# Performance work log

Hardware: AMD Instinct MI355X
Metric: run time of the kernel (lower is better)

## Reference

```python
import jax, jax.numpy as jnp
import numpy as np

NEG = -10000.0
START_ID, END_ID, PAD_ID = 0, 1, 2
B, S, T = 512, 512, 128


def setup_inputs() -> dict:
    key = jax.random.key(0)
    k1, k2, k3, k4 = jax.random.split(key, 4)
    x = jax.random.normal(k1, (B, S, T), dtype=jnp.float32)
    tags = jax.random.randint(k2, (B, S), 0, T)
    # prefix-ones mask; lengths in [1, S-2] so the gather at mask.sum(1) is in-range
    lengths = jax.random.randint(k3, (B,), 1, S - 1)
    mask = (jnp.arange(S)[None, :] < lengths[:, None]).astype(jnp.float32)
    # torch xavier_normal_ on (T, T): std = sqrt(2 / (T + T))
    std = (2.0 / (T + T)) ** 0.5
    transition = std * jax.random.normal(k4, (T, T), dtype=jnp.float32)
    return {"x": x, "tags": tags, "mask": mask, "transition": transition}


def _crf_forward(x, mask, transition):
    # forward algorithm: log partition function, shape (B,)
    b, s, t = x.shape
    alpha0 = jnp.full((b, t), NEG, dtype=x.dtype).at[:, START_ID].set(0.0)

    def step(alpha, inp):
        x_t, m_t = inp  # (B,T), (B,)
        # scores[b, next, prev] = alpha[b, prev] + x_t[b, next] + transition[next, prev]
        scores = alpha[:, None, :] + x_t[:, :, None] + transition[None, :, :]
        new = jax.scipy.special.logsumexp(scores, axis=2)  # (B,T)
        m = m_t[:, None]
        return new * m + alpha * (1.0 - m), None

    alpha, _ = jax.lax.scan(step, alpha0, (jnp.swapaxes(x, 0, 1), jnp.swapaxes(mask, 0, 1)))
    return jax.scipy.special.logsumexp(alpha + transition[END_ID], axis=1)


def _crf_score(x, tags, mask, transition):
    # gold path score, shape (B,) — emission at t is paired with tags[:, t+1]
    b, s, t = x.shape
    em = jnp.take_along_axis(x[:, : s - 1], tags[:, 1:s, None], axis=2)[..., 0]  # (B,S-1)
    tr = transition[tags[:, 1:s], tags[:, : s - 1]]  # (B,S-1)
    score = jnp.sum((em + tr) * mask[:, : s - 1], axis=1)
    last_idx = mask.sum(axis=1).astype(jnp.int32)  # (B,)
    last_tag = jnp.take_along_axis(tags, last_idx[:, None], axis=1)[:, 0]
    return score + transition[END_ID, last_tag]


def reference(x, tags, mask, transition):
    fwd_score = _crf_forward(x, mask, transition)
    gold_score = _crf_score(x, tags, mask, transition)
    return jnp.mean(fwd_score - gold_score)
```

## Files before the change

kernel.cpp:

```cpp
#include <hip/hip_runtime.h>

#define NTAG 128
#define SEQ 512
#define NBATCH 512
#define END_ID 1

typedef _Float16 h2 __attribute__((ext_vector_type(2)));
typedef __fp16 fp16x2 __attribute__((ext_vector_type(2)));
typedef uint u32x32 __attribute__((ext_vector_type(32)));

#define LOG2E 1.4426950408889634f
#define LN2   0.6931471805599453f

__device__ __forceinline__ float bcast0(float v) {
  return __int_as_float(__builtin_amdgcn_readfirstlane(__float_as_int(v)));
}
__device__ __forceinline__ uint pack2(float a, float b) {
  fp16x2 h = __builtin_amdgcn_cvt_pkrtz(a, b);
  return __builtin_bit_cast(uint, h);
}
__device__ __forceinline__ h2 as_h2(uint u) { return __builtin_bit_cast(h2, u); }

__device__ __forceinline__ float fast_exp2(float x) {
#if __has_builtin(__builtin_amdgcn_exp2f)
  return __builtin_amdgcn_exp2f(x);
#else
  return exp2f(x);
#endif
}
__device__ __forceinline__ float fast_log2(float x) {
#if __has_builtin(__builtin_amdgcn_logf)
  return __builtin_amdgcn_logf(x);
#else
  return log2f(x);
#endif
}

#if __has_builtin(__builtin_amdgcn_fdot2)
#define FDOT2(pu, eu, acc) acc = __builtin_amdgcn_fdot2(as_h2(pu), as_h2(eu), acc, false)
#else
#define FDOT2(pu, eu, acc) do { h2 _p = as_h2(pu), _e = as_h2(eu); \
  acc = fmaf((float)_p.x, (float)_e.x, fmaf((float)_p.y, (float)_e.y, acc)); } while (0)
#endif

__global__ __launch_bounds__(64, 1) void crf_kernel(
    const float* __restrict__ x,
    const int*   __restrict__ tags,
    const float* __restrict__ mask,
    const float* __restrict__ trans,
    float* __restrict__ ws)
{
  const int b    = blockIdx.x;
  const int lane = threadIdx.x;

  const float* xb   = x    + (size_t)b * SEQ * NTAG;
  const float* mrow = mask + (size_t)b * SEQ;
  const int*   trow = tags + (size_t)b * SEQ;

  float msum = 0.f;
  #pragma unroll
  for (int i = 0; i < SEQ / 64; ++i) msum += mrow[lane + i * 64];
  #pragma unroll
  for (int off = 1; off < 64; off <<= 1) msum += __shfl_xor(msum, off);
  const int len = (int)msum;

  u32x32 eL0, eL1, eH0, eH1;
  {
    const float4* r0 = (const float4*)(trans + (size_t)(2 * lane) * NTAG);
    const float4* r1 = (const float4*)(trans + (size_t)(2 * lane + 1) * NTAG);
    #pragma unroll
    for (int k4 = 0; k4 < 16; ++k4) {
      float4 lo = r0[k4], hi = r1[k4];
      eL0[2 * k4 + 0] = pack2(fast_exp2(lo.x * LOG2E), fast_exp2(lo.y * LOG2E));
      eL0[2 * k4 + 1] = pack2(fast_exp2(lo.z * LOG2E), fast_exp2(lo.w * LOG2E));
      eH0[2 * k4 + 0] = pack2(fast_exp2(hi.x * LOG2E), fast_exp2(hi.y * LOG2E));
      eH0[2 * k4 + 1] = pack2(fast_exp2(hi.z * LOG2E), fast_exp2(hi.w * LOG2E));
    }
    #pragma unroll
    for (int k4 = 16; k4 < 32; ++k4) {
      float4 lo = r0[k4], hi = r1[k4];
      eL1[2 * (k4 - 16) + 0] = pack2(fast_exp2(lo.x * LOG2E), fast_exp2(lo.y * LOG2E));
      eL1[2 * (k4 - 16) + 1] = pack2(fast_exp2(lo.z * LOG2E), fast_exp2(lo.w * LOG2E));
      eH1[2 * (k4 - 16) + 0] = pack2(fast_exp2(hi.x * LOG2E), fast_exp2(hi.y * LOG2E));
      eH1[2 * (k4 - 16) + 1] = pack2(fast_exp2(hi.z * LOG2E), fast_exp2(hi.w * LOG2E));
    }
  }

  float A_lo = (lane == 0) ? 0.f : -14427.f;
  float A_hi = -14427.f;
  float2 xt = ((const float2*)xb)[lane];

  for (int t = 0; t < len; ++t) {
    const float M = bcast0(A_lo);
    const uint pk = pack2(fminf(fast_exp2(A_lo - M), 60000.f),
                          fminf(fast_exp2(A_hi - M), 60000.f));

    const float2 xn = ((const float2*)(xb + (size_t)(t + 1) * NTAG))[lane];

    float qL = 0.f, qH = 0.f;
    #pragma unroll
    for (int c = 0; c < 64; ++c) {
      const uint pc = (uint)__builtin_amdgcn_readlane((int)pk, c);
      const uint el = (c < 32) ? eL0[c] : eL1[c - 32];
      const uint eh = (c < 32) ? eH0[c] : eH1[c - 32];
      FDOT2(pc, el, qL);
      FDOT2(pc, eh, qH);
    }

    A_lo = fmaf(xt.x, LOG2E, M + fast_log2(qL));
    A_hi = fmaf(xt.y, LOG2E, M + fast_log2(qH));
    xt = xn;
  }

  const float a_lo = A_lo * LN2;
  const float a_hi = A_hi * LN2;

  const float2 te = ((const float2*)(trans + END_ID * NTAG))[lane];
  const float v_lo = a_lo + te.x;
  const float v_hi = a_hi + te.y;
  float m2 = fmaxf(v_lo, v_hi);
  #pragma unroll
  for (int off = 1; off < 64; off <<= 1) m2 = fmaxf(m2, __shfl_xor(m2, off));
  float s = fast_exp2((v_lo - m2) * LOG2E) + fast_exp2((v_hi - m2) * LOG2E);
  #pragma unroll
  for (int off = 1; off < 64; off <<= 1) s += __shfl_xor(s, off);
  const float fwd = m2 + fast_log2(s) * LN2;

  float g = 0.f;
  for (int i = lane; i < len; i += 64) {
    const int tn = trow[i + 1];
    const int tp = trow[i];
    g += xb[(size_t)i * NTAG + tn] + trans[tn * NTAG + tp];
  }
  #pragma unroll
  for (int off = 1; off < 64; off <<= 1) g += __shfl_xor(g, off);

  if (lane == 0) {
    const float gold = g + trans[END_ID * NTAG + trow[len]];
    ws[b] = fwd - gold;
  }
}

__global__ void reduce_kernel(const float* __restrict__ ws, float* __restrict__ out) {
  __shared__ float sm[8];
  const int tid = threadIdx.x;
  float v = ws[tid];
  #pragma unroll
  for (int off = 1; off < 64; off <<= 1) v += __shfl_xor(v, off);
  if ((tid & 63) == 0) sm[tid >> 6] = v;
  __syncthreads();
  if (tid == 0) {
    float s = 0.f;
    #pragma unroll
    for (int w = 0; w < 8; ++w) s += sm[w];
    out[0] = s * (1.0f / 512.0f);
  }
}

extern "C" void kernel_launch(void* const* d_in, const int* in_sizes, int n_in,
                              void* d_out, int out_size, void* d_ws, size_t ws_size,
                              hipStream_t stream) {
  const float* x     = (const float*)d_in[0];
  const int*   tags  = (const int*)d_in[1];
  const float* mask  = (const float*)d_in[2];
  const float* trans = (const float*)d_in[3];
  float*       ws    = (float*)d_ws;

  crf_kernel<<<NBATCH, 64, 0, stream>>>(x, tags, mask, trans, ws);
  reduce_kernel<<<1, 512, 0, stream>>>(ws, (float*)d_out);
}
```

Baseline: 386.6 us.

## Split CRF forward recurrence across two waves with LDS-shared probabilities

Each batch row now runs on 128 threads (two wavefronts), one tag per thread, instead of one wavefront handling two tags per lane. The per-step exponentiated alpha vector goes through double-buffered LDS with a block barrier, and the per-wave max offsets are reconciled with an exp2 rescale, replacing the 64 readlane broadcasts. This halves the per-thread dot-product work and the transition-matrix register footprint on the serial critical path. In exchange it adds a __syncthreads, LDS writes and reads on every time step, plus extra barriers in the final reductions.

```diff
diff --git a/kernel.cpp b/kernel.cpp
--- a/kernel.cpp
+++ b/kernel.cpp
@@ -43,7 +43,7 @@
   acc = fmaf((float)_p.x, (float)_e.x, fmaf((float)_p.y, (float)_e.y, acc)); } while (0)
 #endif
 
-__global__ __launch_bounds__(64, 1) void crf_kernel(
+__global__ __launch_bounds__(128, 1) void crf_kernel(
     const float* __restrict__ x,
     const int*   __restrict__ tags,
     const float* __restrict__ mask,
@@ -51,7 +51,13 @@
     float* __restrict__ ws)
 {
   const int b    = blockIdx.x;
-  const int lane = threadIdx.x;
+  const int tid  = threadIdx.x;
+  const int lane = tid & 63;
+  const int wv   = tid >> 6;
+
+  __shared__ alignas(16) _Float16 p_lds[2][NTAG];
+  __shared__ float m_lds[2][2];
+  __shared__ float red[4];
 
   const float* xb   = x    + (size_t)b * SEQ * NTAG;
   const float* mrow = mask + (size_t)b * SEQ;
@@ -59,84 +65,101 @@
 
   float msum = 0.f;
   #pragma unroll
-  for (int i = 0; i < SEQ / 64; ++i) msum += mrow[lane + i * 64];
+  for (int i = 0; i < SEQ / 128; ++i) msum += mrow[tid + i * 128];
   #pragma unroll
   for (int off = 1; off < 64; off <<= 1) msum += __shfl_xor(msum, off);
-  const int len = (int)msum;
+  if (lane == 0) red[wv] = msum;
+  __syncthreads();
+  const int len = (int)(red[0] + red[1]);
+  __syncthreads();
 
-  u32x32 eL0, eL1, eH0, eH1;
+  u32x32 eA, eB;
   {
-    const float4* r0 = (const float4*)(trans + (size_t)(2 * lane) * NTAG);
-    const float4* r1 = (const float4*)(trans + (size_t)(2 * lane + 1) * NTAG);
+    const float4* r = (const float4*)(trans + (size_t)tid * NTAG);
     #pragma unroll
     for (int k4 = 0; k4 < 16; ++k4) {
-      float4 lo = r0[k4], hi = r1[k4];
-      eL0[2 * k4 + 0] = pack2(fast_exp2(lo.x * LOG2E), fast_exp2(lo.y * LOG2E));
-      eL0[2 * k4 + 1] = pack2(fast_exp2(lo.z * LOG2E), fast_exp2(lo.w * LOG2E));
-      eH0[2 * k4 + 0] = pack2(fast_exp2(hi.x * LOG2E), fast_exp2(hi.y * LOG2E));
-      eH0[2 * k4 + 1] = pack2(fast_exp2(hi.z * LOG2E), fast_exp2(hi.w * LOG2E));
+      float4 f = r[k4];
+      eA[2 * k4 + 0] = pack2(fast_exp2(f.x * LOG2E), fast_exp2(f.y * LOG2E));
+      eA[2 * k4 + 1] = pack2(fast_exp2(f.z * LOG2E), fast_exp2(f.w * LOG2E));
     }
     #pragma unroll
     for (int k4 = 16; k4 < 32; ++k4) {
-      float4 lo = r0[k4], hi = r1[k4];
-      eL1[2 * (k4 - 16) + 0] = pack2(fast_exp2(lo.x * LOG2E), fast_exp2(lo.y * LOG2E));
-      eL1[2 * (k4 - 16) + 1] = pack2(fast_exp2(lo.z * LOG2E), fast_exp2(lo.w * LOG2E));
-      eH1[2 * (k4 - 16) + 0] = pack2(fast_exp2(hi.x * LOG2E), fast_exp2(hi.y * LOG2E));
-      eH1[2 * (k4 - 16) + 1] = pack2(fast_exp2(hi.z * LOG2E), fast_exp2(hi.w * LOG2E));
+      float4 f = r[k4];
+      eB[2 * (k4 - 16) + 0] = pack2(fast_exp2(f.x * LOG2E), fast_exp2(f.y * LOG2E));
+      eB[2 * (k4 - 16) + 1] = pack2(fast_exp2(f.z * LOG2E), fast_exp2(f.w * LOG2E));
     }
   }
 
-  float A_lo = (lane == 0) ? 0.f : -14427.f;
-  float A_hi = -14427.f;
-  float2 xt = ((const float2*)xb)[lane];
+  float A  = (tid == 0) ? 0.f : -14427.f;
+  float xt = xb[tid];
 
   for (int t = 0; t < len; ++t) {
-    const float M = bcast0(A_lo);
-    const uint pk = pack2(fminf(fast_exp2(A_lo - M), 60000.f),
-                          fminf(fast_exp2(A_hi - M), 60000.f));
+    const int buf = t & 1;
+    const float Mw = bcast0(A);
+    const float p  = fminf(fast_exp2(A - Mw), 60000.f);
+    p_lds[buf][tid] = (_Float16)p;
+    if (lane == 0) m_lds[buf][wv] = Mw;
 
-    const float2 xn = ((const float2*)(xb + (size_t)(t + 1) * NTAG))[lane];
+    const float xn = xb[(size_t)(t + 1) * NTAG + tid];
 
-    float qL = 0.f, qH = 0.f;
+    __syncthreads();
+
+    const float2 mv = *(const float2*)m_lds[buf];
+    const uint4* p4 = (const uint4*)p_lds[buf];
+
+    float a0 = 0.f, a1 = 0.f, b0 = 0.f, b1 = 0.f;
     #pragma unroll
-    for (int c = 0; c < 64; ++c) {
-      const uint pc = (uint)__builtin_amdgcn_readlane((int)pk, c);
-      const uint el = (c < 32) ? eL0[c] : eL1[c - 32];
-      const uint eh = (c < 32) ? eH0[c] : eH1[c - 32];
-      FDOT2(pc, el, qL);
-      FDOT2(pc, eh, qH);
+    for (int c = 0; c < 8; ++c) {
+      uint4 pv = p4[c];
+      FDOT2(pv.x, eA[4 * c + 0], a0);
+      FDOT2(pv.y, eA[4 * c + 1], a1);
+      FDOT2(pv.z, eA[4 * c + 2], a0);
+      FDOT2(pv.w, eA[4 * c + 3], a1);
     }
-
-    A_lo = fmaf(xt.x, LOG2E, M + fast_log2(qL));
-    A_hi = fmaf(xt.y, LOG2E, M + fast_log2(qH));
+    #pragma unroll
+    for (int c = 8; c < 16; ++c) {
+      uint4 pv = p4[c];
+      FDOT2(pv.x, eB[4 * (c - 8) + 0], b0);
+      FDOT2(pv.y, eB[4 * (c - 8) + 1], b1);
+      FDOT2(pv.z, eB[4 * (c - 8) + 2], b0);
+      FDOT2(pv.w, eB[4 * (c - 8) + 3], b1);
+    }
+    const float q = (a0 + a1) + (b0 + b1) * fast_exp2(mv.y - mv.x);
+    A  = fmaf(xt, LOG2E, mv.x + fast_log2(q));
     xt = xn;
   }
 
-  const float a_lo = A_lo * LN2;
-  const float a_hi = A_hi * LN2;
+  const float a_nat = A * LN2;
 
-  const float2 te = ((const float2*)(trans + END_ID * NTAG))[lane];
-  const float v_lo = a_lo + te.x;
-  const float v_hi = a_hi + te.y;
-  float m2 = fmaxf(v_lo, v_hi);
+  __syncthreads();
+  const float v = a_nat + trans[END_ID * NTAG + tid];
+  float m2 = v;
   #pragma unroll
   for (int off = 1; off < 64; off <<= 1) m2 = fmaxf(m2, __shfl_xor(m2, off));
-  float s = fast_exp2((v_lo - m2) * LOG2E) + fast_exp2((v_hi - m2) * LOG2E);
+  if (lane == 0) red[wv] = m2;
+  __syncthreads();
+  m2 = fmaxf(red[0], red[1]);
+  float s = fast_exp2((v - m2) * LOG2E);
   #pragma unroll
   for (int off = 1; off < 64; off <<= 1) s += __shfl_xor(s, off);
-  const float fwd = m2 + fast_log2(s) * LN2;
+  __syncthreads();
+  if (lane == 0) red[2 + wv] = s;
+  __syncthreads();
+  const float fwd = m2 + fast_log2(red[2] + red[3]) * LN2;
 
   float g = 0.f;
-  for (int i = lane; i < len; i += 64) {
+  for (int i = tid; i < len; i += 128) {
     const int tn = trow[i + 1];
     const int tp = trow[i];
     g += xb[(size_t)i * NTAG + tn] + trans[tn * NTAG + tp];
   }
   #pragma unroll
   for (int off = 1; off < 64; off <<= 1) g += __shfl_xor(g, off);
-
-  if (lane == 0) {
-    const float gold = g + trans[END_ID * NTAG + trow[len]];
+  __syncthreads();
+  if (lane == 0) red[wv] = g;
+  __syncthreads();
+  if (tid == 0) {
+    const float gold = red[0] + red[1] + trans[END_ID * NTAG + trow[len]];
     ws[b] = fwd - gold;
   }
 }
@@ -166,6 +189,6 @@
   const float* trans = (const float*)d_in[3];
   float*       ws    = (float*)d_ws;
 
-  crf_kernel<<<NBATCH, 64, 0, stream>>>(x, tags, mask, trans, ws);
+  crf_kernel<<<NBATCH, 128, 0, stream>>>(x, tags, mask, trans, ws);
   reduce_kernel<<<1, 512, 0, stream>>>(ws, (float*)d_out);
 }
```

Result: slower. 408.2 us (+5.6%).
